# Kernel optimization log

Hardware: AMD Instinct MI355X
Metric: run time of the kernel (lower is better)

## Reference

```python
import jax, jax.numpy as jnp
import numpy as np

V, E, HD, B, T, K = 50000, 256, 512, 64, 512, 16
H = HD // 2            # per-direction LSTM hidden size
START_IDX, STOP_IDX = K - 2, K - 1
NEG = -10000.0


def setup_inputs() -> dict:
    key = jax.random.key(0)
    ks = jax.random.split(key, 12)
    s = 0.05
    sentence = jax.random.randint(ks[0], (B, T), 0, V)
    emb = jax.random.normal(ks[1], (V, E), jnp.float32)
    w_ih_f = jax.random.normal(ks[2], (4 * H, E), jnp.float32) * s
    w_hh_f = jax.random.normal(ks[3], (4 * H, H), jnp.float32) * s
    b_f = jax.random.normal(ks[4], (4 * H,), jnp.float32) * s
    w_ih_b = jax.random.normal(ks[5], (4 * H, E), jnp.float32) * s
    w_hh_b = jax.random.normal(ks[6], (4 * H, H), jnp.float32) * s
    b_b = jax.random.normal(ks[7], (4 * H,), jnp.float32) * s
    w_out = jax.random.normal(ks[8], (K, HD), jnp.float32) * s
    b_out = jax.random.normal(ks[9], (K,), jnp.float32) * s
    transitions = jax.random.normal(ks[10], (K, K), jnp.float32)
    transitions = transitions.at[START_IDX, :].set(NEG)  # nothing transitions into START
    transitions = transitions.at[:, STOP_IDX].set(NEG)   # nothing transitions out of STOP
    return dict(sentence=sentence, emb=emb, w_ih_f=w_ih_f, w_hh_f=w_hh_f, b_f=b_f,
                w_ih_b=w_ih_b, w_hh_b=w_hh_b, b_b=b_b, w_out=w_out, b_out=b_out,
                transitions=transitions)


def _lstm(xs, w_ih, w_hh, b):
    # xs: [T, B, E] -> hs: [T, B, H]; PyTorch gate order i,f,g,o; bias b = b_ih + b_hh
    Bn = xs.shape[1]
    def step(carry, x):
        h, c = carry
        g = x @ w_ih.T + h @ w_hh.T + b
        i, f, gg, o = jnp.split(g, 4, axis=-1)
        c = jax.nn.sigmoid(f) * c + jax.nn.sigmoid(i) * jnp.tanh(gg)
        h = jax.nn.sigmoid(o) * jnp.tanh(c)
        return (h, c), h
    init = (jnp.zeros((Bn, H), xs.dtype), jnp.zeros((Bn, H), xs.dtype))
    return jax.lax.scan(step, init, xs)[1]


def _lstm_feats(sentence, emb, w_ih_f, w_hh_f, b_f, w_ih_b, w_hh_b, b_b, w_out, b_out):
    x = emb[sentence].transpose(1, 0, 2)                 # [T, B, E]
    hf = _lstm(x, w_ih_f, w_hh_f, b_f)                   # forward direction
    hb = _lstm(x[::-1], w_ih_b, w_hh_b, b_b)[::-1]       # backward direction
    h = jnp.concatenate([hf, hb], axis=-1)               # [T, B, HD]
    return h @ w_out.T + b_out                           # [T, B, K]


def _viterbi(feats, transitions):
    # feats: [T, B, K]
    Bn = feats.shape[1]
    init = jnp.full((Bn, K), NEG, jnp.float32).at[:, START_IDX].set(0.0)
    def vstep(fv, feat):
        scores = fv[:, None, :] + transitions[None, :, :]  # [B, next, prev]
        return jnp.max(scores, axis=2) + feat, jnp.argmax(scores, axis=2)
    fv, bptrs = jax.lax.scan(vstep, init, feats)           # bptrs: [T, B, K]
    terminal = fv + transitions[STOP_IDX][None, :]
    best_score = jnp.max(terminal, axis=1)                 # [B]
    best_tag = jnp.argmax(terminal, axis=1)                # [B]
    def bstep(tag, bptr):
        prev = jnp.take_along_axis(bptr, tag[:, None], axis=1)[:, 0]
        return prev, tag
    _, path = jax.lax.scan(bstep, best_tag, bptrs, reverse=True)  # [T, B]
    return best_score, path


def reference(sentence, emb, w_ih_f, w_hh_f, b_f, w_ih_b, w_hh_b, b_b, w_out, b_out, transitions):
    feats = _lstm_feats(sentence, emb, w_ih_f, w_hh_f, b_f, w_ih_b, w_hh_b, b_b, w_out, b_out)
    score, tag_seq = _viterbi(feats, transitions)
    return score, tag_seq
```

## Files before the change

kernel.cpp:

```cpp
#include <hip/hip_runtime.h>
#include <math.h>

typedef _Float16 h2_t  __attribute__((ext_vector_type(2)));
typedef _Float16 h8_t  __attribute__((ext_vector_type(8)));
typedef _Float16 h32_t __attribute__((ext_vector_type(32)));
typedef float    f4_t  __attribute__((ext_vector_type(4)));

#define T_ 512
#define B_ 64
#define E_ 256
#define H_ 256
#define G_ 1024
#define K_ 16
#define NEG_ (-10000.0f)
#define START_ 14
#define STOP_ 15

#if defined(__has_builtin)
#if __has_builtin(__builtin_amdgcn_fdot2)
#define HAVE_FDOT2 1
#endif
#endif

static __device__ __forceinline__ float dot2(h2_t a, h2_t b, float c) {
#ifdef HAVE_FDOT2
    return __builtin_amdgcn_fdot2(a, b, c, false);
#else
    return fmaf((float)a[0], (float)b[0], fmaf((float)a[1], (float)b[1], c));
#endif
}

template <int P, typename V>
static __device__ __forceinline__ h2_t get2(V v) {
    return __builtin_shufflevector(v, v, 2 * P, 2 * P + 1);
}

__global__ __launch_bounds__(256)
void prep_weights(const float* __restrict__ w_hh_f,
                  const float* __restrict__ w_hh_b,
                  const float* __restrict__ w_ih_f,
                  const float* __restrict__ w_ih_b,
                  _Float16* __restrict__ wreg2,
                  _Float16* __restrict__ wih16)
{
    const int blk = blockIdx.x, tid = threadIdx.x;
    if (blk < 64) {
        int e = blk * 256 + tid;
        int q = e & 511;
        int g = e >> 9;
        int d2 = g >> 3, v = g & 7;
        int dir = d2 >> 1, half = d2 & 1;
        int row = (q >> 7) * 256 + half * 128 + (q & 127);
        const float* src = (dir ? w_hh_b : w_hh_f) + (size_t)row * 256 + v * 32;
        _Float16* dst = wreg2 + (size_t)e * 32;
        #pragma unroll
        for (int i = 0; i < 32; ++i) dst[i] = (_Float16)src[i];
    } else {
        int idx = (blk - 64) * 256 + tid;
        int dir = idx / 32768, rem = idx % 32768;
        const float* src = (dir ? w_ih_b : w_ih_f) + (size_t)rem * 8;
        _Float16* dst = wih16 + (size_t)idx * 8;
        #pragma unroll
        for (int i = 0; i < 8; ++i) dst[i] = (_Float16)src[i];
    }
}

__global__ __launch_bounds__(256)
void gates_mfma(const int* __restrict__ sentence,
                const float* __restrict__ emb,
                const _Float16* __restrict__ wih16,
                _Float16* __restrict__ gin_f,
                _Float16* __restrict__ gin_b)
{
    __shared__ _Float16 As[64 * 264];
    __shared__ _Float16 Bs[256 * 40];
    __shared__ int sidx[64];

    const int bm  = blockIdx.x;
    const int dir = blockIdx.y;
    const int tid = threadIdx.x;

    const _Float16* __restrict__ wih = wih16 + (size_t)dir * 262144;
    _Float16* __restrict__ gout      = dir ? gin_b : gin_f;

    if (tid < 64) sidx[tid] = sentence[tid * T_ + bm];
    __syncthreads();

    {
        const int r = tid & 63, kq = tid >> 6;
        const float4* src = (const float4*)(emb + (size_t)sidx[r] * 256 + kq * 64);
        _Float16* dst = As + r * 264 + kq * 64;
        #pragma unroll
        for (int c = 0; c < 8; ++c) {
            float4 v0 = src[2 * c], v1 = src[2 * c + 1];
            h8_t o;
            o[0] = (_Float16)v0.x; o[1] = (_Float16)v0.y;
            o[2] = (_Float16)v0.z; o[3] = (_Float16)v0.w;
            o[4] = (_Float16)v1.x; o[5] = (_Float16)v1.y;
            o[6] = (_Float16)v1.z; o[7] = (_Float16)v1.w;
            *(h8_t*)(dst + c * 8) = o;
        }
    }

    const int wave = tid >> 6, lane = tid & 63;
    const int l15 = lane & 15, quad = lane >> 4;

    for (int pass = 0; pass < 4; ++pass) {
        const int n0 = pass * 256;
        f4_t acc[16];
        #pragma unroll
        for (int nt = 0; nt < 16; ++nt) acc[nt] = (f4_t){0.f, 0.f, 0.f, 0.f};

        for (int kc = 0; kc < 8; ++kc) {
            __syncthreads();
            {
                const h8_t* bsrc = (const h8_t*)(wih + (size_t)(n0 + tid) * 256 + kc * 32);
                #pragma unroll
                for (int c = 0; c < 4; ++c)
                    *(h8_t*)(Bs + tid * 40 + c * 8) = bsrc[c];
            }
            __syncthreads();
            h8_t a = *(const h8_t*)(As + (wave * 16 + l15) * 264 + kc * 32 + quad * 8);
            #pragma unroll
            for (int nt = 0; nt < 16; ++nt) {
                h8_t b = *(const h8_t*)(Bs + (nt * 16 + l15) * 40 + quad * 8);
                acc[nt] = __builtin_amdgcn_mfma_f32_16x16x32_f16(a, b, acc[nt], 0, 0, 0);
            }
        }

        const size_t mbase = (size_t)bm * 64 + wave * 16 + quad * 4;
        #pragma unroll
        for (int nt = 0; nt < 16; ++nt) {
            const int col = n0 + nt * 16 + l15;
            #pragma unroll
            for (int r = 0; r < 4; ++r)
                gout[(mbase + r) * 1024 + col] = (_Float16)acc[nt][r];
        }
    }
}

#define DOT8(W, P0, HV, ACC) do {                                   \
    ACC = dot2(get2<(P0)+0>(W), get2<0>(HV), ACC);                  \
    ACC = dot2(get2<(P0)+1>(W), get2<1>(HV), ACC);                  \
    ACC = dot2(get2<(P0)+2>(W), get2<2>(HV), ACC);                  \
    ACC = dot2(get2<(P0)+3>(W), get2<3>(HV), ACC);                  \
} while (0)

#define VBLK(W, VI) do {                                            \
    h8_t hv0 = HB[(VI)*4+0], hv1 = HB[(VI)*4+1];                    \
    h8_t hv2 = HB[(VI)*4+2], hv3 = HB[(VI)*4+3];                    \
    DOT8(W, 0,  hv0, a0); DOT8(W, 4,  hv1, a1);                     \
    DOT8(W, 8,  hv2, a2); DOT8(W, 12, hv3, a3);                     \
} while (0)

__global__ __attribute__((amdgpu_flat_work_group_size(512, 512),
                          amdgpu_waves_per_eu(2, 2)))
void lstm_pair(const _Float16* __restrict__ gin_f,
               const _Float16* __restrict__ gin_b,
               const _Float16* __restrict__ wreg2,
               const float* __restrict__ b_f,
               const float* __restrict__ b_b,
               float* __restrict__ hf, float* __restrict__ hb,
               unsigned int* __restrict__ hex)
{
    __shared__ h8_t  hbuf8[32];
    __shared__ float gbuf[512];

    const int bid  = blockIdx.x;
    const int c16  = bid >> 4;
    const int w16  = bid & 15;
    const int half = w16 >> 3;
    const int pair = c16 * 8 + (w16 & 7);
    const int dir  = pair >> 6;
    const int b    = pair & 63;
    const int q    = threadIdx.x;

    const int gcl = q >> 7, off = q & 127;
    const int row = gcl * 256 + half * 128 + off;

    const _Float16* __restrict__ gin  = dir ? gin_b : gin_f;
    const float*    __restrict__ bs   = dir ? b_b : b_f;
    float*          __restrict__ hout = dir ? hb : hf;

    const h32_t* wr = (const h32_t*)wreg2 + (size_t)(dir * 2 + half) * 4096 + q;
    h32_t W0 = wr[0 * 512], W1 = wr[1 * 512], W2 = wr[2 * 512], W3 = wr[3 * 512];
    h32_t W4 = wr[4 * 512], W5 = wr[5 * 512], W6 = wr[6 * 512], W7 = wr[7 * 512];

    const float bias = bs[row];

    if (q < 32) hbuf8[q] = (h8_t)(_Float16)0.f;
    float c = 0.f;
    __syncthreads();

    const long tstr = 64 * 1024;
    const long hstr = 64 * 256;
    const int  t0   = dir ? (T_ - 1) : 0;
    const _Float16* gp = gin + (size_t)t0 * tstr + (size_t)b * 1024 + row;
    float*          hp = hout + (size_t)t0 * hstr + (size_t)b * 256 + half * 128 + q;
    const long gstep = dir ? -tstr : tstr;
    const long hstep = dir ? -hstr : hstr;

    unsigned int* hexPub = hex + (size_t)pair * 65536 + (size_t)half * 64 + (q >> 1);
    const int pi = (q >= 128 && q < 192) ? (q - 128) : 0;
    const unsigned int* hexPoll =
        hex + (size_t)pair * 65536 + (size_t)(1 - half) * 64 + pi;
    const int pdst = (1 - half) * 64 + pi;

    const h8_t* HB = hbuf8;
    unsigned int* hbufU = (unsigned int*)hbuf8;
    _Float16*    hbufH = (_Float16*)hbuf8;

    _Float16 gc0 = gp[0];

    for (int s = 0; s < T_; ++s) {
        _Float16 gn0 = gp[gstep];

        float a0 = 0.f, a1 = 0.f, a2 = 0.f, a3 = 0.f;
        VBLK(W0, 0); VBLK(W1, 1); VBLK(W2, 2); VBLK(W3, 3);
        VBLK(W4, 4); VBLK(W5, 5); VBLK(W6, 6); VBLK(W7, 7);

        gbuf[q] = bias + (float)gc0 + ((a0 + a1) + (a2 + a3));
        __syncthreads();

        if (q < 128) {
            float gi = gbuf[q], gf = gbuf[128 + q];
            float gg = gbuf[256 + q], go = gbuf[384 + q];
            float si = 1.f / (1.f + expf(-gi));
            float sf = 1.f / (1.f + expf(-gf));
            float so = 1.f / (1.f + expf(-go));
            c = sf * c + si * tanhf(gg);
            float h = so * tanhf(c);
            hp[0] = h;
            hbufH[half * 128 + q] = (_Float16)h;
            if (s < T_ - 1) {
                float hn = __shfl_down(h, 1, 64);
                if ((q & 1) == 0) {
                    h2_t pk; pk[0] = (_Float16)h; pk[1] = (_Float16)hn;
                    __hip_atomic_store(hexPub + s * 128,
                                       __builtin_bit_cast(unsigned int, pk),
                                       __ATOMIC_RELAXED, __HIP_MEMORY_SCOPE_AGENT);
                }
            }
        } else if (q < 192 && s < T_ - 1) {
            const unsigned int* src = hexPoll + s * 128;
            unsigned int u;
            int guard = 0;
            do {
                u = __hip_atomic_load(src, __ATOMIC_RELAXED,
                                      __HIP_MEMORY_SCOPE_AGENT);
            } while (u == 0xFFFFFFFFu && ++guard < (1 << 20));
            hbufU[pdst] = u;
        }
        gc0 = gn0;
        gp += gstep;
        hp += hstep;
        __syncthreads();
    }
}

__global__ __launch_bounds__(256)
void feats_proj(const float* __restrict__ hf, const float* __restrict__ hb,
                const float* __restrict__ w_out, const float* __restrict__ b_out,
                float* __restrict__ feats)
{
    const int lane = threadIdx.x & 63;
    const int wv   = threadIdx.x >> 6;
    const int m    = blockIdx.x * 4 + wv;
    const int o    = lane & 15;
    const int qq   = lane >> 4;

    const float* hsrc = (qq < 2) ? (hf + (size_t)m * 256 + qq * 128)
                                 : (hb + (size_t)m * 256 + (qq - 2) * 128);
    const float4* h4 = (const float4*)hsrc;
    const float4* w4 = (const float4*)(w_out + o * 512 + qq * 128);

    float acc = 0.f;
    #pragma unroll
    for (int i = 0; i < 32; ++i) {
        float4 hv = h4[i], wvv = w4[i];
        acc = fmaf(hv.x, wvv.x, acc);
        acc = fmaf(hv.y, wvv.y, acc);
        acc = fmaf(hv.z, wvv.z, acc);
        acc = fmaf(hv.w, wvv.w, acc);
    }
    acc += __shfl_xor(acc, 16, 64);
    acc += __shfl_xor(acc, 32, 64);
    if (lane < 16) feats[(size_t)m * 16 + o] = acc + b_out[o];
}

__global__ __launch_bounds__(64)
void viterbi(const float* __restrict__ feats, const float* __restrict__ trans,
             float* __restrict__ out)
{
    __shared__ unsigned char bp[T_][16];
    const int b    = blockIdx.x;
    const int lane = threadIdx.x;
    const int l15  = lane & 15;

    float tr[16];
    #pragma unroll
    for (int p = 0; p < 16; ++p)
        tr[p] = (lane < 16) ? trans[lane * 16 + p] : 0.f;

    float fv = (lane == START_) ? 0.f : NEG_;

    for (int t4 = 0; t4 < T_; t4 += 4) {
        float fblk = feats[((size_t)(t4 + (lane >> 4)) * 64 + b) * 16 + l15];
        #pragma unroll
        for (int tt = 0; tt < 4; ++tt) {
            const int t = t4 + tt;
            float best = -3.4e38f; int arg = 0;
            #pragma unroll
            for (int p = 0; p < 16; ++p) {
                float s = __shfl(fv, p, 64) + tr[p];
                if (s > best) { best = s; arg = p; }
            }
            float ft = __shfl(fblk, tt * 16 + l15, 64);
            if (lane < 16) {
                fv = best + ft;
                bp[t][lane] = (unsigned char)arg;
            }
        }
    }

    float term = fv + ((lane < 16) ? trans[STOP_ * 16 + lane] : 0.f);
    float v  = (lane < 16) ? term : -3.4e38f;
    int  idx = (lane < 16) ? lane : (1 << 20);
    #pragma unroll
    for (int off = 1; off < 64; off <<= 1) {
        float v2 = __shfl_xor(v, off, 64);
        int   i2 = __shfl_xor(idx, off, 64);
        if (v2 > v || (v2 == v && i2 < idx)) { v = v2; idx = i2; }
    }
    __syncthreads();
    if (lane == 0) {
        out[b] = v;
        int tag = idx;
        for (int t = T_ - 1; t >= 0; --t) {
            out[64 + (size_t)t * 64 + b] = (float)tag;
            tag = bp[t][tag];
        }
    }
}

extern "C" void kernel_launch(void* const* d_in, const int* in_sizes, int n_in,
                              void* d_out, int out_size, void* d_ws, size_t ws_size,
                              hipStream_t stream) {
    const int*   sentence = (const int*)d_in[0];
    const float* emb      = (const float*)d_in[1];
    const float* w_ih_f   = (const float*)d_in[2];
    const float* w_hh_f   = (const float*)d_in[3];
    const float* b_f      = (const float*)d_in[4];
    const float* w_ih_b   = (const float*)d_in[5];
    const float* w_hh_b   = (const float*)d_in[6];
    const float* b_b      = (const float*)d_in[7];
    const float* w_out    = (const float*)d_in[8];
    const float* b_out    = (const float*)d_in[9];
    const float* trans    = (const float*)d_in[10];
    float* out = (float*)d_out;

    _Float16* gin_f = (_Float16*)d_ws;
    _Float16* gin_b = gin_f + (size_t)T_ * B_ * G_;
    float* hf    = (float*)(gin_b + (size_t)T_ * B_ * G_);
    float* hb    = hf + (size_t)T_ * B_ * H_;
    float* feats = hb + (size_t)T_ * B_ * H_;
    _Float16* wih16 = (_Float16*)(feats + (size_t)T_ * B_ * K_);
    _Float16* wreg2 = wih16 + 524288;
    unsigned int* hex = (unsigned int*)(wreg2 + 524288);

    prep_weights<<<320, 256, 0, stream>>>(w_hh_f, w_hh_b, w_ih_f, w_ih_b,
                                          wreg2, wih16);
    gates_mfma<<<dim3(512, 2), 256, 0, stream>>>(sentence, emb, wih16,
                                                 gin_f, gin_b);
    hipMemsetAsync(hex, 0xFF, (size_t)33554432, stream);
    lstm_pair<<<256, 512, 0, stream>>>(gin_f, gin_b, wreg2, b_f, b_b,
                                       hf, hb, hex);
    feats_proj<<<8192, 256, 0, stream>>>(hf, hb, w_out, b_out, feats);
    viterbi<<<64, 64, 0, stream>>>(feats, trans, out);
}
```

Baseline: 1.371 ms.

## Overlap partner hidden-state exchange with own-half recurrent matvec

Reorders the recurrent weight columns so each block first multiplies against its own half of h, which is available locally, and only then against the partner block's half. Polling for the partner's published h now happens during the own-half dot products rather than in a separate phase after the gates, so inter-block communication latency is hidden behind compute. An extra barrier is added mid-step, and an asm constraint pins the weight registers. The atomic publish is now issued before the global h store.

```diff
diff --git a/kernel.cpp b/kernel.cpp
--- a/kernel.cpp
+++ b/kernel.cpp
@@ -51,7 +51,9 @@
         int d2 = g >> 3, v = g & 7;
         int dir = d2 >> 1, half = d2 & 1;
         int row = (q >> 7) * 256 + half * 128 + (q & 127);
-        const float* src = (dir ? w_hh_b : w_hh_f) + (size_t)row * 256 + v * 32;
+        int kb  = (v < 4) ? (half * 128 + v * 32)
+                          : ((1 - half) * 128 + (v - 4) * 32);
+        const float* src = (dir ? w_hh_b : w_hh_f) + (size_t)row * 256 + kb;
         _Float16* dst = wreg2 + (size_t)e * 32;
         #pragma unroll
         for (int i = 0; i < 32; ++i) dst[i] = (_Float16)src[i];
@@ -146,9 +148,9 @@
     ACC = dot2(get2<(P0)+3>(W), get2<3>(HV), ACC);                  \
 } while (0)
 
-#define VBLK(W, VI) do {                                            \
-    h8_t hv0 = HB[(VI)*4+0], hv1 = HB[(VI)*4+1];                    \
-    h8_t hv2 = HB[(VI)*4+2], hv3 = HB[(VI)*4+3];                    \
+#define VBLK(W, HBASE, VI) do {                                     \
+    h8_t hv0 = (HBASE)[(VI)*4+0], hv1 = (HBASE)[(VI)*4+1];          \
+    h8_t hv2 = (HBASE)[(VI)*4+2], hv3 = (HBASE)[(VI)*4+3];          \
     DOT8(W, 0,  hv0, a0); DOT8(W, 4,  hv1, a1);                     \
     DOT8(W, 8,  hv2, a2); DOT8(W, 12, hv3, a3);                     \
 } while (0)
@@ -201,23 +203,43 @@
     const long hstep = dir ? -hstr : hstr;
 
     unsigned int* hexPub = hex + (size_t)pair * 65536 + (size_t)half * 64 + (q >> 1);
-    const int pi = (q >= 128 && q < 192) ? (q - 128) : 0;
+    const int pollw = (q >= 128 && q < 192);
+    const int pi = pollw ? (q - 128) : 0;
     const unsigned int* hexPoll =
         hex + (size_t)pair * 65536 + (size_t)(1 - half) * 64 + pi;
     const int pdst = (1 - half) * 64 + pi;
 
-    const h8_t* HB = hbuf8;
+    const h8_t* HBo = hbuf8 + half * 16;
+    const h8_t* HBp = hbuf8 + (1 - half) * 16;
     unsigned int* hbufU = (unsigned int*)hbuf8;
     _Float16*    hbufH = (_Float16*)hbuf8;
 
     _Float16 gc0 = gp[0];
 
     for (int s = 0; s < T_; ++s) {
+        asm volatile("" : "+v"(W0), "+v"(W1), "+v"(W2), "+v"(W3),
+                          "+v"(W4), "+v"(W5), "+v"(W6), "+v"(W7));
+
         _Float16 gn0 = gp[gstep];
 
+        unsigned int u = 0xFFFFFFFFu;
+        if (pollw && s > 0)
+            u = __hip_atomic_load(hexPoll + (size_t)(s - 1) * 128,
+                                  __ATOMIC_RELAXED, __HIP_MEMORY_SCOPE_AGENT);
+
         float a0 = 0.f, a1 = 0.f, a2 = 0.f, a3 = 0.f;
-        VBLK(W0, 0); VBLK(W1, 1); VBLK(W2, 2); VBLK(W3, 3);
-        VBLK(W4, 4); VBLK(W5, 5); VBLK(W6, 6); VBLK(W7, 7);
+        VBLK(W0, HBo, 0); VBLK(W1, HBo, 1); VBLK(W2, HBo, 2); VBLK(W3, HBo, 3);
+
+        if (pollw && s > 0) {
+            int guard = 0;
+            while (u == 0xFFFFFFFFu && ++guard < (1 << 20))
+                u = __hip_atomic_load(hexPoll + (size_t)(s - 1) * 128,
+                                      __ATOMIC_RELAXED, __HIP_MEMORY_SCOPE_AGENT);
+            hbufU[pdst] = u;
+        }
+        __syncthreads();
+
+        VBLK(W4, HBp, 0); VBLK(W5, HBp, 1); VBLK(W6, HBp, 2); VBLK(W7, HBp, 3);
 
         gbuf[q] = bias + (float)gc0 + ((a0 + a1) + (a2 + a3));
         __syncthreads();
@@ -230,26 +252,17 @@
             float so = 1.f / (1.f + expf(-go));
             c = sf * c + si * tanhf(gg);
             float h = so * tanhf(c);
-            hp[0] = h;
-            hbufH[half * 128 + q] = (_Float16)h;
             if (s < T_ - 1) {
                 float hn = __shfl_down(h, 1, 64);
                 if ((q & 1) == 0) {
                     h2_t pk; pk[0] = (_Float16)h; pk[1] = (_Float16)hn;
-                    __hip_atomic_store(hexPub + s * 128,
+                    __hip_atomic_store(hexPub + (size_t)s * 128,
                                        __builtin_bit_cast(unsigned int, pk),
                                        __ATOMIC_RELAXED, __HIP_MEMORY_SCOPE_AGENT);
                 }
             }
-        } else if (q < 192 && s < T_ - 1) {
-            const unsigned int* src = hexPoll + s * 128;
-            unsigned int u;
-            int guard = 0;
-            do {
-                u = __hip_atomic_load(src, __ATOMIC_RELAXED,
-                                      __HIP_MEMORY_SCOPE_AGENT);
-            } while (u == 0xFFFFFFFFu && ++guard < (1 << 20));
-            hbufU[pdst] = u;
+            hp[0] = h;
+            hbufH[half * 128 + q] = (_Float16)h;
         }
         gc0 = gn0;
         gp += gstep;
```

New measurement: 1.379 ms. About the same (+0.6%).

## Replace per-sequence fdot2 LSTM recurrence with batched MFMA recurrence across blocks

Applied to the files above, without the earlier changes.

The recurrent LSTM kernel no longer assigns each batch row to a pair of blocks doing fdot2 matrix-vector products. Instead it launches 128 blocks. Each block owns an 8-hidden-unit slice (32 gate rows) for 32 batch rows of one direction, holds its W_hh fragments in registers, and computes the recurrent product with 16x16x32 MFMA. Every block publishes its fp16 h slice to a global mailbox each step and polls all 128 slices from its peers, so the recurrence becomes a tensor-core GEMM. In exchange, each step now needs an all-to-all exchange across 32 blocks per group, which costs more global polling traffic and tighter cross-block synchronisation. The weight prep kernel is changed to produce the new fragment layout.

```diff
diff --git a/kernel.cpp b/kernel.cpp
--- a/kernel.cpp
+++ b/kernel.cpp
@@ -2,8 +2,8 @@
 #include <math.h>
 
 typedef _Float16 h2_t  __attribute__((ext_vector_type(2)));
+typedef _Float16 h4_t  __attribute__((ext_vector_type(4)));
 typedef _Float16 h8_t  __attribute__((ext_vector_type(8)));
-typedef _Float16 h32_t __attribute__((ext_vector_type(32)));
 typedef float    f4_t  __attribute__((ext_vector_type(4)));
 
 #define T_ 512
@@ -16,47 +16,36 @@
 #define START_ 14
 #define STOP_ 15
 
-#if defined(__has_builtin)
-#if __has_builtin(__builtin_amdgcn_fdot2)
-#define HAVE_FDOT2 1
-#endif
-#endif
-
-static __device__ __forceinline__ float dot2(h2_t a, h2_t b, float c) {
-#ifdef HAVE_FDOT2
-    return __builtin_amdgcn_fdot2(a, b, c, false);
-#else
-    return fmaf((float)a[0], (float)b[0], fmaf((float)a[1], (float)b[1], c));
-#endif
-}
-
-template <int P, typename V>
-static __device__ __forceinline__ h2_t get2(V v) {
-    return __builtin_shufflevector(v, v, 2 * P, 2 * P + 1);
-}
-
 __global__ __launch_bounds__(256)
 void prep_weights(const float* __restrict__ w_hh_f,
                   const float* __restrict__ w_hh_b,
                   const float* __restrict__ w_ih_f,
                   const float* __restrict__ w_ih_b,
-                  _Float16* __restrict__ wreg2,
+                  _Float16* __restrict__ wreg3,
                   _Float16* __restrict__ wih16)
 {
     const int blk = blockIdx.x, tid = threadIdx.x;
-    if (blk < 64) {
-        int e = blk * 256 + tid;
-        int q = e & 511;
-        int g = e >> 9;
-        int d2 = g >> 3, v = g & 7;
-        int dir = d2 >> 1, half = d2 & 1;
-        int row = (q >> 7) * 256 + half * 128 + (q & 127);
-        const float* src = (dir ? w_hh_b : w_hh_f) + (size_t)row * 256 + v * 32;
-        _Float16* dst = wreg2 + (size_t)e * 32;
-        #pragma unroll
-        for (int i = 0; i < 32; ++i) dst[i] = (_Float16)src[i];
+    if (blk < 32) {
+        int idx  = blk * 256 + tid;
+        int dir  = idx >> 12;
+        int j    = (idx >> 7) & 31;
+        int mt   = (idx >> 6) & 1;
+        int lane = idx & 63;
+        int m_local = mt * 16 + (lane & 15);
+        int grow = (m_local >> 3) * 256 + 8 * j + (m_local & 7);
+        int k0   = (lane >> 4) * 8;
+        const float* whh = dir ? w_hh_b : w_hh_f;
+        h8_t* dstb = (h8_t*)wreg3;
+        #pragma unroll
+        for (int kt = 0; kt < 8; ++kt) {
+            const float* src = whh + (size_t)grow * 256 + kt * 32 + k0;
+            h8_t o;
+            #pragma unroll
+            for (int e = 0; e < 8; ++e) o[e] = (_Float16)src[e];
+            dstb[((size_t)(idx >> 6) * 8 + kt) * 64 + lane] = o;
+        }
     } else {
-        int idx = (blk - 64) * 256 + tid;
+        int idx = (blk - 32) * 256 + tid;
         int dir = idx / 32768, rem = idx % 32768;
         const float* src = (dir ? w_ih_b : w_ih_f) + (size_t)rem * 8;
         _Float16* dst = wih16 + (size_t)idx * 8;
@@ -139,122 +128,131 @@
     }
 }
 
-#define DOT8(W, P0, HV, ACC) do {                                   \
-    ACC = dot2(get2<(P0)+0>(W), get2<0>(HV), ACC);                  \
-    ACC = dot2(get2<(P0)+1>(W), get2<1>(HV), ACC);                  \
-    ACC = dot2(get2<(P0)+2>(W), get2<2>(HV), ACC);                  \
-    ACC = dot2(get2<(P0)+3>(W), get2<3>(HV), ACC);                  \
-} while (0)
-
-#define VBLK(W, VI) do {                                            \
-    h8_t hv0 = HB[(VI)*4+0], hv1 = HB[(VI)*4+1];                    \
-    h8_t hv2 = HB[(VI)*4+2], hv3 = HB[(VI)*4+3];                    \
-    DOT8(W, 0,  hv0, a0); DOT8(W, 4,  hv1, a1);                     \
-    DOT8(W, 8,  hv2, a2); DOT8(W, 12, hv3, a3);                     \
-} while (0)
-
-__global__ __attribute__((amdgpu_flat_work_group_size(512, 512),
-                          amdgpu_waves_per_eu(2, 2)))
-void lstm_pair(const _Float16* __restrict__ gin_f,
+__global__ __launch_bounds__(256)
+void lstm_gemm(const _Float16* __restrict__ gin_f,
                const _Float16* __restrict__ gin_b,
-               const _Float16* __restrict__ wreg2,
+               const _Float16* __restrict__ wreg3,
                const float* __restrict__ b_f,
                const float* __restrict__ b_b,
                float* __restrict__ hf, float* __restrict__ hb,
-               unsigned int* __restrict__ hex)
-{
-    __shared__ h8_t  hbuf8[32];
-    __shared__ float gbuf[512];
-
-    const int bid  = blockIdx.x;
-    const int c16  = bid >> 4;
-    const int w16  = bid & 15;
-    const int half = w16 >> 3;
-    const int pair = c16 * 8 + (w16 & 7);
-    const int dir  = pair >> 6;
-    const int b    = pair & 63;
-    const int q    = threadIdx.x;
-
-    const int gcl = q >> 7, off = q & 127;
-    const int row = gcl * 256 + half * 128 + off;
+               unsigned int* __restrict__ mail)
+{
+    __shared__ _Float16 hbufT[8192];
+    __shared__ float    gbuf[32 * 34];
+
+    const int bid = blockIdx.x;
+    const int g   = bid & 3;
+    const int j   = bid >> 2;
+    const int dir = g >> 1, bh = g & 1;
+    const int t   = threadIdx.x;
+    const int wv  = t >> 6, lane = t & 63;
+    const int mt  = wv >> 1, nt = wv & 1;
+    const int l15 = lane & 15, quad = lane >> 4;
 
     const _Float16* __restrict__ gin  = dir ? gin_b : gin_f;
     const float*    __restrict__ bs   = dir ? b_b : b_f;
     float*          __restrict__ hout = dir ? hb : hf;
 
-    const h32_t* wr = (const h32_t*)wreg2 + (size_t)(dir * 2 + half) * 4096 + q;
-    h32_t W0 = wr[0 * 512], W1 = wr[1 * 512], W2 = wr[2 * 512], W3 = wr[3 * 512];
-    h32_t W4 = wr[4 * 512], W5 = wr[5 * 512], W6 = wr[6 * 512], W7 = wr[7 * 512];
-
-    const float bias = bs[row];
-
-    if (q < 32) hbuf8[q] = (h8_t)(_Float16)0.f;
+    const h8_t* wsrc = (const h8_t*)wreg3 +
+                       ((((size_t)dir * 32 + j) * 2 + mt) * 8) * 64 + lane;
+    h8_t Afr[8];
+    #pragma unroll
+    for (int kt = 0; kt < 8; ++kt) Afr[kt] = wsrc[kt * 64];
+
+    const int mq = mt * 16 + quad * 4;
+    const int growBase = (mq >> 3) * 256 + 8 * j + (mq & 7);
+    const f4_t bias4 = *(const f4_t*)(bs + growBase);
+
+    const int sdir = dir ? -1 : 1;
+    const int s0   = dir ? (T_ - 1) : 0;
+    const _Float16* gp = gin + (size_t)s0 * 65536 +
+                         (size_t)(bh * 32 + nt * 16 + l15) * 1024 + growBase;
+    const long gstep = (long)sdir * 65536;
+
+    const int n32 = t & 31;
+    const int rl  = t >> 5;
+    float* hp = hout + ((size_t)s0 * 64 + bh * 32 + n32) * 256 + 8 * j + rl;
+    const long hstep = (long)sdir * (64 * 256);
+
+    unsigned int* mailG = mail + (size_t)g * (512 * 128 * 32);
+    const int kp0 = t >> 5;
+    unsigned int* hbU = (unsigned int*)hbufT;
+
+    #pragma unroll
+    for (int i = 0; i < 16; ++i) {
+        int kp  = kp0 + 8 * i;
+        int off = (((n32 >> 4) * 8 + (kp >> 4)) * 4 + ((kp >> 2) & 3)) * 64 +
+                  (n32 & 15) * 4 + (kp & 3);
+        hbU[off] = 0u;
+    }
     float c = 0.f;
     __syncthreads();
 
-    const long tstr = 64 * 1024;
-    const long hstr = 64 * 256;
-    const int  t0   = dir ? (T_ - 1) : 0;
-    const _Float16* gp = gin + (size_t)t0 * tstr + (size_t)b * 1024 + row;
-    float*          hp = hout + (size_t)t0 * hstr + (size_t)b * 256 + half * 128 + q;
-    const long gstep = dir ? -tstr : tstr;
-    const long hstep = dir ? -hstr : hstr;
-
-    unsigned int* hexPub = hex + (size_t)pair * 65536 + (size_t)half * 64 + (q >> 1);
-    const int pi = (q >= 128 && q < 192) ? (q - 128) : 0;
-    const unsigned int* hexPoll =
-        hex + (size_t)pair * 65536 + (size_t)(1 - half) * 64 + pi;
-    const int pdst = (1 - half) * 64 + pi;
-
-    const h8_t* HB = hbuf8;
-    unsigned int* hbufU = (unsigned int*)hbuf8;
-    _Float16*    hbufH = (_Float16*)hbuf8;
-
-    _Float16 gc0 = gp[0];
-
     for (int s = 0; s < T_; ++s) {
-        _Float16 gn0 = gp[gstep];
-
-        float a0 = 0.f, a1 = 0.f, a2 = 0.f, a3 = 0.f;
-        VBLK(W0, 0); VBLK(W1, 1); VBLK(W2, 2); VBLK(W3, 3);
-        VBLK(W4, 4); VBLK(W5, 5); VBLK(W6, 6); VBLK(W7, 7);
-
-        gbuf[q] = bias + (float)gc0 + ((a0 + a1) + (a2 + a3));
+        h4_t g4 = *(const h4_t*)gp;
+
+        if (s > 0) {
+            const unsigned int* pb = mailG + (size_t)(s - 1) * 4096 +
+                                     kp0 * 32 + n32;
+            unsigned int uv[16];
+            #pragma unroll
+            for (int i = 0; i < 16; ++i)
+                uv[i] = __hip_atomic_load(pb + i * 256, __ATOMIC_RELAXED,
+                                          __HIP_MEMORY_SCOPE_AGENT);
+            #pragma unroll
+            for (int i = 0; i < 16; ++i) {
+                unsigned int u = uv[i];
+                int guard = 0;
+                while (u == 0xFFFFFFFFu && ++guard < (1 << 20))
+                    u = __hip_atomic_load(pb + i * 256, __ATOMIC_RELAXED,
+                                          __HIP_MEMORY_SCOPE_AGENT);
+                int kp  = kp0 + 8 * i;
+                int off = (((n32 >> 4) * 8 + (kp >> 4)) * 4 +
+                           ((kp >> 2) & 3)) * 64 + (n32 & 15) * 4 + (kp & 3);
+                hbU[off] = u;
+            }
+        }
         __syncthreads();
 
-        if (q < 128) {
-            float gi = gbuf[q], gf = gbuf[128 + q];
-            float gg = gbuf[256 + q], go = gbuf[384 + q];
+        f4_t acc;
+        acc[0] = bias4[0] + (float)g4[0];
+        acc[1] = bias4[1] + (float)g4[1];
+        acc[2] = bias4[2] + (float)g4[2];
+        acc[3] = bias4[3] + (float)g4[3];
+        #pragma unroll
+        for (int kt = 0; kt < 8; ++kt) {
+            h8_t bf = *(const h8_t*)(hbufT + ((nt * 8 + kt) << 9) + (lane << 3));
+            acc = __builtin_amdgcn_mfma_f32_16x16x32_f16(Afr[kt], bf, acc, 0, 0, 0);
+        }
+
+        const int nl = nt * 16 + l15;
+        gbuf[(mq + 0) * 34 + nl] = acc[0];
+        gbuf[(mq + 1) * 34 + nl] = acc[1];
+        gbuf[(mq + 2) * 34 + nl] = acc[2];
+        gbuf[(mq + 3) * 34 + nl] = acc[3];
+        __syncthreads();
+
+        {
+            float gi = gbuf[(0 * 8 + rl) * 34 + n32];
+            float gf = gbuf[(1 * 8 + rl) * 34 + n32];
+            float gg = gbuf[(2 * 8 + rl) * 34 + n32];
+            float go = gbuf[(3 * 8 + rl) * 34 + n32];
             float si = 1.f / (1.f + expf(-gi));
             float sf = 1.f / (1.f + expf(-gf));
             float so = 1.f / (1.f + expf(-go));
             c = sf * c + si * tanhf(gg);
             float h = so * tanhf(c);
             hp[0] = h;
-            hbufH[half * 128 + q] = (_Float16)h;
-            if (s < T_ - 1) {
-                float hn = __shfl_down(h, 1, 64);
-                if ((q & 1) == 0) {
-                    h2_t pk; pk[0] = (_Float16)h; pk[1] = (_Float16)hn;
-                    __hip_atomic_store(hexPub + s * 128,
-                                       __builtin_bit_cast(unsigned int, pk),
-                                       __ATOMIC_RELAXED, __HIP_MEMORY_SCOPE_AGENT);
-                }
-            }
-        } else if (q < 192 && s < T_ - 1) {
-            const unsigned int* src = hexPoll + s * 128;
-            unsigned int u;
-            int guard = 0;
-            do {
-                u = __hip_atomic_load(src, __ATOMIC_RELAXED,
-                                      __HIP_MEMORY_SCOPE_AGENT);
-            } while (u == 0xFFFFFFFFu && ++guard < (1 << 20));
-            hbufU[pdst] = u;
-        }
-        gc0 = gn0;
+            float hn = __shfl_down(h, 32, 64);
+            if ((t & 32) == 0 && s < T_ - 1) {
+                h2_t pk; pk[0] = (_Float16)h; pk[1] = (_Float16)hn;
+                __hip_atomic_store(mailG + ((size_t)s * 128 + 4 * j + wv) * 32 + n32,
+                                   __builtin_bit_cast(unsigned int, pk),
+                                   __ATOMIC_RELAXED, __HIP_MEMORY_SCOPE_AGENT);
+            }
+        }
         gp += gstep;
         hp += hstep;
-        __syncthreads();
     }
 }
 
@@ -365,16 +363,16 @@
     float* hb    = hf + (size_t)T_ * B_ * H_;
     float* feats = hb + (size_t)T_ * B_ * H_;
     _Float16* wih16 = (_Float16*)(feats + (size_t)T_ * B_ * K_);
-    _Float16* wreg2 = wih16 + 524288;
-    unsigned int* hex = (unsigned int*)(wreg2 + 524288);
-
-    prep_weights<<<320, 256, 0, stream>>>(w_hh_f, w_hh_b, w_ih_f, w_ih_b,
-                                          wreg2, wih16);
+    _Float16* wreg3 = wih16 + 524288;
+    unsigned int* mail = (unsigned int*)(wreg3 + 524288);
+
+    prep_weights<<<288, 256, 0, stream>>>(w_hh_f, w_hh_b, w_ih_f, w_ih_b,
+                                          wreg3, wih16);
     gates_mfma<<<dim3(512, 2), 256, 0, stream>>>(sentence, emb, wih16,
                                                  gin_f, gin_b);
-    hipMemsetAsync(hex, 0xFF, (size_t)33554432, stream);
-    lstm_pair<<<256, 512, 0, stream>>>(gin_f, gin_b, wreg2, b_f, b_b,
-                                       hf, hb, hex);
+    hipMemsetAsync(mail, 0xFF, (size_t)33554432, stream);
+    lstm_gemm<<<128, 256, 0, stream>>>(gin_f, gin_b, wreg3, b_f, b_b,
+                                       hf, hb, mail);
     feats_proj<<<8192, 256, 0, stream>>>(hf, hb, w_out, b_out, feats);
     viterbi<<<64, 64, 0, stream>>>(feats, trans, out);
 }
```

Result: slower. 3.201 ms (+133.5%).
